# Performance work log

Hardware: AMD Instinct MI355X
Metric: run time of the kernel (lower is better)

## Reference

```python
import jax, jax.numpy as jnp
import numpy as np
import math

B, T, H, C = 256, 512, 1024, 10


def setup_inputs() -> dict:
    key = jax.random.key(0)
    k_x, k_whx, k_whh, k_wph = jax.random.split(key, 4)
    stdv = 1.0 / math.sqrt(H)
    x = jax.random.normal(k_x, (B, T), dtype=jnp.float32)
    whx = jax.random.uniform(k_whx, (H, 1), minval=-stdv, maxval=stdv, dtype=jnp.float32)
    whh = jax.random.uniform(k_whh, (H, H), minval=-stdv, maxval=stdv, dtype=jnp.float32)
    bias_h = jnp.zeros((H,), dtype=jnp.float32)
    wph = jax.random.uniform(k_wph, (C, H), minval=-stdv, maxval=stdv, dtype=jnp.float32)
    bias_p = jnp.zeros((C,), dtype=jnp.float32)
    return {"x": x, "whx": whx, "whh": whh, "bias_h": bias_h, "wph": wph, "bias_p": bias_p}


def reference(x, whx, whh, bias_h, wph, bias_p):
    # x: [B, T]; per-step input is scalar (input_dim == 1)
    batch = x.shape[0]
    h0 = jnp.zeros((batch, whh.shape[0]), dtype=x.dtype)

    def step(h_prev, x_t):
        # x_t: [B] -> [B,1] @ [1,H] ; h_prev @ whh.T : [B,H]
        h = jnp.tanh(x_t[:, None] @ whx.T + h_prev @ whh.T + bias_h)
        return h, None

    h_last, _ = jax.lax.scan(step, h0, x.T)  # scan over time, xs: [T, B]
    p = h_last @ wph.T + bias_p  # [B, C]
    return p
```

## Files before the change

kernel.cpp:

```cpp
#include <hip/hip_runtime.h>
#include <hip/hip_bf16.h>

#define TT 512
#define HH 1024
#define CC 10
#define GROUPS 16
#define MEMBERS 8
#define SLOT_BYTES (GROUPS * 32768)

typedef __bf16 bf16x8 __attribute__((ext_vector_type(8)));
typedef float  f32x4  __attribute__((ext_vector_type(4)));

#define SENT64 0x7F7F7F7F7F7F7F7Full

__device__ __forceinline__ float tanh_poly(float z) {
    float z2 = z * z;
    float c = fmaf(z2, fmaf(z2, fmaf(z2, -17.f / 315.f, 2.f / 15.f), -1.f / 3.f), 1.f);
    return z * c;
}

__device__ __forceinline__ void load_tile(unsigned long long base, unsigned o,
    uint4& a0, uint4& a1, uint4& a2, uint4& a3,
    uint4& a4, uint4& a5, uint4& a6, uint4& a7)
{
    unsigned o0 = o, o1 = o + 4096u, o2 = o + 8192u, o3 = o + 12288u,
             o4 = o + 16384u, o5 = o + 20480u, o6 = o + 24576u, o7 = o + 28672u;
    asm volatile(
        "global_load_dwordx4 %0, %8, %16 sc0 sc1\n\t"
        "global_load_dwordx4 %1, %9, %16 sc0 sc1\n\t"
        "global_load_dwordx4 %2, %10, %16 sc0 sc1\n\t"
        "global_load_dwordx4 %3, %11, %16 sc0 sc1\n\t"
        "global_load_dwordx4 %4, %12, %16 sc0 sc1\n\t"
        "global_load_dwordx4 %5, %13, %16 sc0 sc1\n\t"
        "global_load_dwordx4 %6, %14, %16 sc0 sc1\n\t"
        "global_load_dwordx4 %7, %15, %16 sc0 sc1\n\t"
        "s_waitcnt vmcnt(0)"
        : "=&v"(a0), "=&v"(a1), "=&v"(a2), "=&v"(a3),
          "=&v"(a4), "=&v"(a5), "=&v"(a6), "=&v"(a7)
        : "v"(o0), "v"(o1), "v"(o2), "v"(o3),
          "v"(o4), "v"(o5), "v"(o6), "v"(o7), "s"(base)
        : "memory");
}

__device__ __forceinline__ unsigned sent_bits(unsigned v) {
    unsigned x = v ^ 0x7F7F7F7Fu;
    return (x - 0x00010001u) & ~x & 0x80008000u;
}
__device__ __forceinline__ unsigned quad_sent(const uint4& v) {
    return sent_bits(v.x) | sent_bits(v.y) | sent_bits(v.z) | sent_bits(v.w);
}

__global__ __launch_bounds__(256, 1)
void rnn_persistent(const float* __restrict__ x, const float* __restrict__ whx,
                    const float* __restrict__ whh, const float* __restrict__ bias_h,
                    const float* __restrict__ wph, const float* __restrict__ bias_p,
                    float* __restrict__ out, char* __restrict__ ws)
{
    __shared__ __bf16 hs[2][16384];
    __shared__ __bf16 stg[2048];
    __shared__ float  xs[TT * 16];

    const int tid = threadIdx.x;
    const int b   = blockIdx.x;
    const int group  = b >> 3;
    const int member = b & 7;
    const int rbase  = group * 16;

    const int wave = tid >> 6;
    const int lane = tid & 63;
    const int n = lane & 15;
    const int q = lane >> 4;
    const int jb = member * 128 + wave * 32;

    for (int e = tid; e < 16 * TT; e += 256) {
        int r = e >> 9, t = e & (TT - 1);
        xs[t * 16 + r] = x[(size_t)(rbase + r) * TT + t];
    }

    bf16x8 Bf[2][32];
    #pragma unroll
    for (int ct = 0; ct < 2; ++ct) {
        const float* wrow = whh + (size_t)(jb + ct * 16 + n) * HH + q * 8;
        #pragma unroll
        for (int kt = 0; kt < 32; ++kt) {
            const float* p = wrow + kt * 32;
            bf16x8 v;
            #pragma unroll
            for (int u = 0; u < 8; ++u) v[u] = (__bf16)p[u];
            Bf[ct][kt] = v;
        }
    }
    float whx_l[2], bh_l[2];
    whx_l[0] = whx[jb + n];      bh_l[0] = bias_h[jb + n];
    whx_l[1] = whx[jb + 16 + n]; bh_l[1] = bias_h[jb + 16 + n];

    const unsigned long long tileoff = (unsigned long long)group * 32768ull;
    const unsigned obase = (unsigned)(tid * 16);

    __syncthreads();

    for (int s = 0; s < TT; ++s) {
        const unsigned long long gb =
            (unsigned long long)(ws + (size_t)(s & 3) * SLOT_BYTES) + tileoff;
        uint4 g0, g1, g2, g3, g4, g5, g6, g7;
        for (;;) {
            load_tile(gb, obase, g0, g1, g2, g3, g4, g5, g6, g7);
            unsigned bad = quad_sent(g0) | quad_sent(g1) | quad_sent(g2) | quad_sent(g3)
                         | quad_sent(g4) | quad_sent(g5) | quad_sent(g6) | quad_sent(g7);
            if (__all(bad == 0u)) break;
        }

        {
            char* hp = (char*)hs[s & 1] + tid * 16;
            *(uint4*)(hp)          = g0;
            *(uint4*)(hp + 4096)   = g1;
            *(uint4*)(hp + 8192)   = g2;
            *(uint4*)(hp + 12288)  = g3;
            *(uint4*)(hp + 16384)  = g4;
            *(uint4*)(hp + 20480)  = g5;
            *(uint4*)(hp + 24576)  = g6;
            *(uint4*)(hp + 28672)  = g7;
        }

        {
            unsigned long long* rst = (unsigned long long*)
                (ws + (size_t)((s + 2) & 3) * SLOT_BYTES + tileoff
                    + (size_t)member * 4096) + (size_t)tid * 2;
            __hip_atomic_store(rst,     SENT64, __ATOMIC_RELAXED, __HIP_MEMORY_SCOPE_AGENT);
            __hip_atomic_store(rst + 1, SENT64, __ATOMIC_RELAXED, __HIP_MEMORY_SCOPE_AGENT);
        }

        __syncthreads();

        f32x4 acc0 = (f32x4){0.f, 0.f, 0.f, 0.f};
        f32x4 acc1 = (f32x4){0.f, 0.f, 0.f, 0.f};
        const __bf16* hp = hs[s & 1];
        #pragma unroll
        for (int kt = 0; kt < 32; ++kt) {
            bf16x8 a = *(const bf16x8*)&hp[kt * 512 + lane * 8];
            acc0 = __builtin_amdgcn_mfma_f32_16x16x32_bf16(a, Bf[0][kt], acc0, 0, 0, 0);
            acc1 = __builtin_amdgcn_mfma_f32_16x16x32_bf16(a, Bf[1][kt], acc1, 0, 0, 0);
        }

        #pragma unroll
        for (int ct = 0; ct < 2; ++ct) {
            f32x4 tot = ct ? acc1 : acc0;
            #pragma unroll
            for (int i = 0; i < 4; ++i) {
                int r = q * 4 + i;
                float z = tot[i] + xs[s * 16 + r] * whx_l[ct] + bh_l[ct];
                stg[wave * 512 + (ct * 256 + (n >> 3) * 128) + r * 8 + (n & 7)] =
                    (__bf16)tanh_poly(z);
            }
        }

        asm volatile("s_waitcnt vmcnt(0)" ::: "memory");
        {
            unsigned long long v0 = *(const unsigned long long*)&stg[tid * 8];
            unsigned long long v1 = *(const unsigned long long*)&stg[tid * 8 + 4];
            unsigned long long* dstq = (unsigned long long*)
                (ws + (size_t)((s + 1) & 3) * SLOT_BYTES + tileoff
                    + (size_t)member * 4096) + (size_t)tid * 2;
            __hip_atomic_store(dstq,     v0, __ATOMIC_RELAXED, __HIP_MEMORY_SCOPE_AGENT);
            __hip_atomic_store(dstq + 1, v1, __ATOMIC_RELAXED, __HIP_MEMORY_SCOPE_AGENT);
        }
    }

    if (member == 0) {
        const unsigned long long gb = (unsigned long long)ws + tileoff;
        uint4 g0, g1, g2, g3, g4, g5, g6, g7;
        for (;;) {
            load_tile(gb, obase, g0, g1, g2, g3, g4, g5, g6, g7);
            unsigned bad = quad_sent(g0) | quad_sent(g1) | quad_sent(g2) | quad_sent(g3)
                         | quad_sent(g4) | quad_sent(g5) | quad_sent(g6) | quad_sent(g7);
            if (__all(bad == 0u)) break;
        }
        {
            char* hp = (char*)hs[0] + tid * 16;
            *(uint4*)(hp)          = g0;
            *(uint4*)(hp + 4096)   = g1;
            *(uint4*)(hp + 8192)   = g2;
            *(uint4*)(hp + 12288)  = g3;
            *(uint4*)(hp + 16384)  = g4;
            *(uint4*)(hp + 20480)  = g5;
            *(uint4*)(hp + 24576)  = g6;
            *(uint4*)(hp + 28672)  = g7;
        }
        __syncthreads();

        if (tid < 16 * CC) {
            int r = tid / CC, c = tid % CC;
            const float* wr = wph + (size_t)c * HH;
            float sum = 0.f;
            for (int kt = 0; kt < 32; ++kt)
                #pragma unroll
                for (int qq = 0; qq < 4; ++qq) {
                    bf16x8 hv = *(const bf16x8*)&hs[0][kt * 512 + (qq * 16 + r) * 8];
                    const float* wp = wr + kt * 32 + qq * 8;
                    #pragma unroll
                    for (int u = 0; u < 8; ++u) sum += (float)hv[u] * wp[u];
                }
            out[(rbase + r) * CC + c] = sum + bias_p[c];
        }
    }
}

extern "C" void kernel_launch(void* const* d_in, const int* in_sizes, int n_in,
                              void* d_out, int out_size, void* d_ws, size_t ws_size,
                              hipStream_t stream) {
    const float* x      = (const float*)d_in[0];
    const float* whx    = (const float*)d_in[1];
    const float* whh    = (const float*)d_in[2];
    const float* bias_h = (const float*)d_in[3];
    const float* wph    = (const float*)d_in[4];
    const float* bias_p = (const float*)d_in[5];
    float* out = (float*)d_out;

    (void)hipMemsetAsync(d_ws, 0, SLOT_BYTES, stream);
    (void)hipMemsetAsync((char*)d_ws + SLOT_BYTES, 0x7F, 3 * (size_t)SLOT_BYTES, stream);

    rnn_persistent<<<dim3(GROUPS * MEMBERS), dim3(256), 0, stream>>>(
        x, whx, whh, bias_h, wph, bias_p, out, (char*)d_ws);
}
```

Before: 1.580 ms.

## Stream h tile per wave directly into MFMA registers with chunked readiness polling

Each wave now loads the full 16-row h tile itself from global memory in eight 4 KB chunks, checks each chunk for sentinels, and runs its MFMAs on a chunk as soon as that chunk is ready. This removes the LDS staging of h, the block-wide __syncthreads, and the all-or-nothing retry of the whole tile. The sentinel reset moves to the end of the step, targeting slot s+3 instead of s+2. In exchange each wave issues four times as many global loads per step and re-polls chunks that are not yet ready, with a short sleep when a pass makes no progress.

```diff
diff --git a/kernel.cpp b/kernel.cpp
--- a/kernel.cpp
+++ b/kernel.cpp
@@ -6,6 +6,7 @@
 #define CC 10
 #define GROUPS 16
 #define MEMBERS 8
+#define NBLK (GROUPS * MEMBERS)
 #define SLOT_BYTES (GROUPS * 32768)
 
 typedef __bf16 bf16x8 __attribute__((ext_vector_type(8)));
@@ -17,6 +18,63 @@
     float z2 = z * z;
     float c = fmaf(z2, fmaf(z2, fmaf(z2, -17.f / 315.f, 2.f / 15.f), -1.f / 3.f), 1.f);
     return z * c;
+}
+
+__device__ __forceinline__ unsigned sent_bits(unsigned v) {
+    unsigned x = v ^ 0x7F7F7F7Fu;
+    return (x - 0x00010001u) & ~x & 0x80008000u;
+}
+__device__ __forceinline__ unsigned quad_sent(const uint4& v) {
+    return sent_bits(v.x) | sent_bits(v.y) | sent_bits(v.z) | sent_bits(v.w);
+}
+
+#define VMWAIT0()                                                             \
+    do {                                                                      \
+        asm volatile("s_waitcnt vmcnt(0)" ::: "memory");                      \
+        __builtin_amdgcn_sched_barrier(0);                                    \
+    } while (0)
+
+#define IW4(off, r0, r1, r2, r3)                                              \
+    do {                                                                      \
+        asm volatile(                                                         \
+            "global_load_dwordx4 %0, %4, %5 sc0 sc1\n\t"                      \
+            "global_load_dwordx4 %1, %4, %5 offset:1024 sc0 sc1\n\t"          \
+            "global_load_dwordx4 %2, %4, %5 offset:2048 sc0 sc1\n\t"          \
+            "global_load_dwordx4 %3, %4, %5 offset:3072 sc0 sc1\n\t"          \
+            "s_waitcnt vmcnt(4)"                                              \
+            : "=&v"(r0), "=&v"(r1), "=&v"(r2), "=&v"(r3)                      \
+            : "v"(off), "s"(gb) : "memory");                                  \
+        __builtin_amdgcn_sched_barrier(0);                                    \
+    } while (0)
+
+#define CHK(c, r0, r1, r2, r3)                                                \
+    if (mask & (1u << (c))) {                                                 \
+        unsigned bad = quad_sent(r0) | quad_sent(r1)                          \
+                     | quad_sent(r2) | quad_sent(r3);                         \
+        if (__all(bad == 0u)) {                                               \
+            mfma_chunk<(c)>(r0, r1, r2, r3, Bf, acc0, acc1);                  \
+            nm &= ~(1u << (c));                                               \
+        }                                                                     \
+    }
+
+template<int C>
+__device__ __forceinline__ void mfma_chunk(
+    const uint4& p0, const uint4& p1, const uint4& p2, const uint4& p3,
+    const bf16x8 (&Bf)[2][32], f32x4& a0, f32x4& a1)
+{
+    bf16x8 x0, x1, x2, x3;
+    __builtin_memcpy(&x0, &p0, 16);
+    __builtin_memcpy(&x1, &p1, 16);
+    __builtin_memcpy(&x2, &p2, 16);
+    __builtin_memcpy(&x3, &p3, 16);
+    a0 = __builtin_amdgcn_mfma_f32_16x16x32_bf16(x0, Bf[0][4*C+0], a0, 0, 0, 0);
+    a1 = __builtin_amdgcn_mfma_f32_16x16x32_bf16(x0, Bf[1][4*C+0], a1, 0, 0, 0);
+    a0 = __builtin_amdgcn_mfma_f32_16x16x32_bf16(x1, Bf[0][4*C+1], a0, 0, 0, 0);
+    a1 = __builtin_amdgcn_mfma_f32_16x16x32_bf16(x1, Bf[1][4*C+1], a1, 0, 0, 0);
+    a0 = __builtin_amdgcn_mfma_f32_16x16x32_bf16(x2, Bf[0][4*C+2], a0, 0, 0, 0);
+    a1 = __builtin_amdgcn_mfma_f32_16x16x32_bf16(x2, Bf[1][4*C+2], a1, 0, 0, 0);
+    a0 = __builtin_amdgcn_mfma_f32_16x16x32_bf16(x3, Bf[0][4*C+3], a0, 0, 0, 0);
+    a1 = __builtin_amdgcn_mfma_f32_16x16x32_bf16(x3, Bf[1][4*C+3], a1, 0, 0, 0);
 }
 
 __device__ __forceinline__ void load_tile(unsigned long long base, unsigned o,
@@ -42,21 +100,13 @@
         : "memory");
 }
 
-__device__ __forceinline__ unsigned sent_bits(unsigned v) {
-    unsigned x = v ^ 0x7F7F7F7Fu;
-    return (x - 0x00010001u) & ~x & 0x80008000u;
-}
-__device__ __forceinline__ unsigned quad_sent(const uint4& v) {
-    return sent_bits(v.x) | sent_bits(v.y) | sent_bits(v.z) | sent_bits(v.w);
-}
-
 __global__ __launch_bounds__(256, 1)
 void rnn_persistent(const float* __restrict__ x, const float* __restrict__ whx,
                     const float* __restrict__ whh, const float* __restrict__ bias_h,
                     const float* __restrict__ wph, const float* __restrict__ bias_p,
                     float* __restrict__ out, char* __restrict__ ws)
 {
-    __shared__ __bf16 hs[2][16384];
+    __shared__ __bf16 hs[16384];
     __shared__ __bf16 stg[2048];
     __shared__ float  xs[TT * 16];
 
@@ -95,51 +145,31 @@
     whx_l[1] = whx[jb + 16 + n]; bh_l[1] = bias_h[jb + 16 + n];
 
     const unsigned long long tileoff = (unsigned long long)group * 32768ull;
-    const unsigned obase = (unsigned)(tid * 16);
+    const unsigned lo = (unsigned)(lane * 16);
 
     __syncthreads();
 
     for (int s = 0; s < TT; ++s) {
         const unsigned long long gb =
             (unsigned long long)(ws + (size_t)(s & 3) * SLOT_BYTES) + tileoff;
-        uint4 g0, g1, g2, g3, g4, g5, g6, g7;
-        for (;;) {
-            load_tile(gb, obase, g0, g1, g2, g3, g4, g5, g6, g7);
-            unsigned bad = quad_sent(g0) | quad_sent(g1) | quad_sent(g2) | quad_sent(g3)
-                         | quad_sent(g4) | quad_sent(g5) | quad_sent(g6) | quad_sent(g7);
-            if (__all(bad == 0u)) break;
-        }
-
-        {
-            char* hp = (char*)hs[s & 1] + tid * 16;
-            *(uint4*)(hp)          = g0;
-            *(uint4*)(hp + 4096)   = g1;
-            *(uint4*)(hp + 8192)   = g2;
-            *(uint4*)(hp + 12288)  = g3;
-            *(uint4*)(hp + 16384)  = g4;
-            *(uint4*)(hp + 20480)  = g5;
-            *(uint4*)(hp + 24576)  = g6;
-            *(uint4*)(hp + 28672)  = g7;
-        }
-
-        {
-            unsigned long long* rst = (unsigned long long*)
-                (ws + (size_t)((s + 2) & 3) * SLOT_BYTES + tileoff
-                    + (size_t)member * 4096) + (size_t)tid * 2;
-            __hip_atomic_store(rst,     SENT64, __ATOMIC_RELAXED, __HIP_MEMORY_SCOPE_AGENT);
-            __hip_atomic_store(rst + 1, SENT64, __ATOMIC_RELAXED, __HIP_MEMORY_SCOPE_AGENT);
-        }
-
-        __syncthreads();
-
         f32x4 acc0 = (f32x4){0.f, 0.f, 0.f, 0.f};
         f32x4 acc1 = (f32x4){0.f, 0.f, 0.f, 0.f};
-        const __bf16* hp = hs[s & 1];
-        #pragma unroll
-        for (int kt = 0; kt < 32; ++kt) {
-            bf16x8 a = *(const bf16x8*)&hp[kt * 512 + lane * 8];
-            acc0 = __builtin_amdgcn_mfma_f32_16x16x32_bf16(a, Bf[0][kt], acc0, 0, 0, 0);
-            acc1 = __builtin_amdgcn_mfma_f32_16x16x32_bf16(a, Bf[1][kt], acc1, 0, 0, 0);
+
+        unsigned mask = 0xffu;
+        while (mask) {
+            unsigned nm = mask;
+            uint4 a0, a1, a2, a3, b0, b1, b2, b3;
+            IW4(lo +     0u, a0, a1, a2, a3);
+            IW4(lo +  4096u, b0, b1, b2, b3);  CHK(0, a0, a1, a2, a3)
+            IW4(lo +  8192u, a0, a1, a2, a3);  CHK(1, b0, b1, b2, b3)
+            IW4(lo + 12288u, b0, b1, b2, b3);  CHK(2, a0, a1, a2, a3)
+            IW4(lo + 16384u, a0, a1, a2, a3);  CHK(3, b0, b1, b2, b3)
+            IW4(lo + 20480u, b0, b1, b2, b3);  CHK(4, a0, a1, a2, a3)
+            IW4(lo + 24576u, a0, a1, a2, a3);  CHK(5, b0, b1, b2, b3)
+            IW4(lo + 28672u, b0, b1, b2, b3);  CHK(6, a0, a1, a2, a3)
+            VMWAIT0();                         CHK(7, b0, b1, b2, b3)
+            if (nm == mask) __builtin_amdgcn_s_sleep(2);
+            mask = nm;
         }
 
         #pragma unroll
@@ -153,30 +183,38 @@
                     (__bf16)tanh_poly(z);
             }
         }
-
-        asm volatile("s_waitcnt vmcnt(0)" ::: "memory");
+        asm volatile("s_waitcnt lgkmcnt(0)" ::: "memory");
+        __builtin_amdgcn_sched_barrier(0);
+        unsigned long long v0 = *(const unsigned long long*)&stg[tid * 8];
+        unsigned long long v1 = *(const unsigned long long*)&stg[tid * 8 + 4];
+
+        VMWAIT0();
         {
-            unsigned long long v0 = *(const unsigned long long*)&stg[tid * 8];
-            unsigned long long v1 = *(const unsigned long long*)&stg[tid * 8 + 4];
             unsigned long long* dstq = (unsigned long long*)
                 (ws + (size_t)((s + 1) & 3) * SLOT_BYTES + tileoff
                     + (size_t)member * 4096) + (size_t)tid * 2;
             __hip_atomic_store(dstq,     v0, __ATOMIC_RELAXED, __HIP_MEMORY_SCOPE_AGENT);
             __hip_atomic_store(dstq + 1, v1, __ATOMIC_RELAXED, __HIP_MEMORY_SCOPE_AGENT);
+            unsigned long long* rst = (unsigned long long*)
+                (ws + (size_t)((s + 3) & 3) * SLOT_BYTES + tileoff
+                    + (size_t)member * 4096) + (size_t)tid * 2;
+            __hip_atomic_store(rst,     SENT64, __ATOMIC_RELAXED, __HIP_MEMORY_SCOPE_AGENT);
+            __hip_atomic_store(rst + 1, SENT64, __ATOMIC_RELAXED, __HIP_MEMORY_SCOPE_AGENT);
         }
     }
 
     if (member == 0) {
-        const unsigned long long gb = (unsigned long long)ws + tileoff;
+        const unsigned long long gb2 = (unsigned long long)ws + tileoff;
+        const unsigned obase = (unsigned)(tid * 16);
         uint4 g0, g1, g2, g3, g4, g5, g6, g7;
         for (;;) {
-            load_tile(gb, obase, g0, g1, g2, g3, g4, g5, g6, g7);
+            load_tile(gb2, obase, g0, g1, g2, g3, g4, g5, g6, g7);
             unsigned bad = quad_sent(g0) | quad_sent(g1) | quad_sent(g2) | quad_sent(g3)
                          | quad_sent(g4) | quad_sent(g5) | quad_sent(g6) | quad_sent(g7);
             if (__all(bad == 0u)) break;
         }
         {
-            char* hp = (char*)hs[0] + tid * 16;
+            char* hp = (char*)hs + tid * 16;
             *(uint4*)(hp)          = g0;
             *(uint4*)(hp + 4096)   = g1;
             *(uint4*)(hp + 8192)   = g2;
@@ -195,7 +233,7 @@
             for (int kt = 0; kt < 32; ++kt)
                 #pragma unroll
                 for (int qq = 0; qq < 4; ++qq) {
-                    bf16x8 hv = *(const bf16x8*)&hs[0][kt * 512 + (qq * 16 + r) * 8];
+                    bf16x8 hv = *(const bf16x8*)&hs[kt * 512 + (qq * 16 + r) * 8];
                     const float* wp = wr + kt * 32 + qq * 8;
                     #pragma unroll
                     for (int u = 0; u < 8; ++u) sum += (float)hv[u] * wp[u];
@@ -219,6 +257,6 @@
     (void)hipMemsetAsync(d_ws, 0, SLOT_BYTES, stream);
     (void)hipMemsetAsync((char*)d_ws + SLOT_BYTES, 0x7F, 3 * (size_t)SLOT_BYTES, stream);
 
-    rnn_persistent<<<dim3(GROUPS * MEMBERS), dim3(256), 0, stream>>>(
+    rnn_persistent<<<dim3(NBLK), dim3(256), 0, stream>>>(
         x, whx, whh, bias_h, wph, bias_p, out, (char*)d_ws);
 }
```

New measurement: 2.340 ms. 48.1% more time.
